# Kernel optimization log

Hardware: AMD Instinct MI355X
Metric: run time of the kernel (lower is better)

## Reference

```python
import jax, jax.numpy as jnp
import numpy as np

B, H, S, D = 4, 16, 1024, 64

def setup_inputs() -> dict:
    key = jax.random.key(0)
    kq, kk, kv, kb, km = jax.random.split(key, 5)
    return {
        "q": jax.random.normal(kq, (B, H, S, D), dtype=jnp.float32),
        "k": jax.random.normal(kk, (B, H, S, D), dtype=jnp.float32),
        "v": jax.random.normal(kv, (B, H, S, D), dtype=jnp.float32),
        "add_attn": jax.random.normal(kb, (B, 1, S, S), dtype=jnp.float32),
        "mask": jax.random.randint(km, (B, 1, 1, S), 0, 2, dtype=jnp.int32),
    }

def reference(q, k, v, add_attn, mask):
    d_emb = q.shape[-1]
    scale = 1.0 / jnp.sqrt(jnp.float32(d_emb)).astype(q.dtype)
    # scores: [B,H,Sq,Sk]
    attn = jnp.einsum('bhqd,bhkd->bhqk', q * scale, k)
    attn = attn + add_attn
    attn = jnp.where(mask == 0, jnp.asarray(-1e9, attn.dtype), attn)
    attn = jax.nn.softmax(attn, axis=-1)  # dropout with p=0 is identity
    output = jnp.einsum('bhqk,bhkd->bhqd', attn, v)
    return (output, attn)
```

## Files before the change

### kernel.cpp

```cpp
#include <hip/hip_runtime.h>
#include <math.h>

#define BB 4
#define HH 16
#define SS 1024
#define DD 64
#define QT 16
#define NKW 4
#define KPW 256
#define HPB 4
#define PTL 264
#define OSTR 68

typedef __attribute__((ext_vector_type(8))) short bf16x8;
typedef __attribute__((ext_vector_type(4))) float f32x4;
typedef __attribute__((ext_vector_type(4))) int   i32x4;

static __device__ inline unsigned short f2bf(float f) {
    unsigned int u = __float_as_uint(f);
    u += 0x7fff + ((u >> 16) & 1);
    return (unsigned short)(u >> 16);
}

__global__ __launch_bounds__(256) void convert_qk(const float* __restrict__ q,
                                                  const float* __restrict__ k,
                                                  unsigned short* __restrict__ qb,
                                                  unsigned short* __restrict__ kb) {
    const int idx = blockIdx.x * 256 + threadIdx.x;
    float4 qv = ((const float4*)q)[idx];
    float4 kv = ((const float4*)k)[idx];
    ushort4 qo = make_ushort4(f2bf(qv.x), f2bf(qv.y), f2bf(qv.z), f2bf(qv.w));
    ushort4 ko = make_ushort4(f2bf(kv.x), f2bf(kv.y), f2bf(kv.z), f2bf(kv.w));
    ((ushort4*)qb)[idx] = qo;
    ((ushort4*)kb)[idx] = ko;
}

__global__ __launch_bounds__(256) void transpose_v(const float* __restrict__ v,
                                                   unsigned short* __restrict__ vt) {
    __shared__ unsigned short t[DD][258];
    const int bh = blockIdx.y;
    const int k0 = blockIdx.x * 256;
    const float* vb = v + ((size_t)bh * SS + k0) * DD;
#pragma unroll
    for (int j = 0; j < 16; ++j) {
        const int f   = j * 256 + threadIdx.x;
        const int row = f >> 4;
        const int d4  = (f & 15) << 2;
        float4 x = ((const float4*)vb)[f];
        t[d4 + 0][row] = f2bf(x.x);
        t[d4 + 1][row] = f2bf(x.y);
        t[d4 + 2][row] = f2bf(x.z);
        t[d4 + 3][row] = f2bf(x.w);
    }
    __syncthreads();
    unsigned short* vo = vt + (size_t)bh * DD * SS + k0;
#pragma unroll
    for (int j = 0; j < 8; ++j) {
        const int f  = j * 256 + threadIdx.x;
        const int d  = f >> 5;
        const int k8 = (f & 31) << 3;
        const unsigned int* lp = (const unsigned int*)&t[d][k8];
        uint4 w;
        w.x = lp[0]; w.y = lp[1]; w.z = lp[2]; w.w = lp[3];
        *(uint4*)(vo + (size_t)d * SS + k8) = w;
    }
}

__global__ __launch_bounds__(256, 2) void attn_mfma(
    const unsigned short* __restrict__ qb,
    const unsigned short* __restrict__ kb,
    const unsigned short* __restrict__ vtb,
    const float* __restrict__ add_attn,
    const int*   __restrict__ mask,
    float* __restrict__ out,
    float* __restrict__ attn_out)
{
    const int P    = blockIdx.x;
    const int xcd  = P & 7;
    const int slot = P >> 3;
    const int hg   = slot & 3;
    const int g    = ((slot >> 2) << 3) | xcd;
    const int qt   = g & 63;
    const int b    = g >> 6;

    const int tid  = threadIdx.x;
    const int wave = tid >> 6;
    const int lane = tid & 63;
    const int col  = lane & 15;
    const int quad = lane >> 4;

    __shared__ unsigned short p_tile[NKW][QT][PTL];
    __shared__ float a_stage[NKW][4][264];
    __shared__ float red_m[NKW][QT];
    __shared__ float red_l[NKW][QT];
    float* o_w = (float*)&p_tile[wave][0][0];

    const int q0  = qt * QT;
    const int wk0 = wave * KPW;

    const float* brow = add_attn + ((size_t)b * SS + q0 + col) * SS;
    const int*   mrow = mask + b * SS;
    float br[16][4];
#pragma unroll
    for (int t = 0; t < 16; ++t) {
        const int kof = wk0 + t * 16 + quad * 4;
        const f32x4 bv = *(const f32x4*)(brow + kof);
        const i32x4 mv = *(const i32x4*)(mrow + kof);
#pragma unroll
        for (int r = 0; r < 4; ++r)
            br[t][r] = mv[r] ? bv[r] : -1e9f;
    }

    for (int hi = 0; hi < HPB; ++hi) {
        const int bh = b * HH + hg * HPB + hi;

        const unsigned short* qrow = qb + ((size_t)bh * SS + q0 + col) * DD + quad * 8;
        const bf16x8 bq0 = *(const bf16x8*)(qrow);
        const bf16x8 bq1 = *(const bf16x8*)(qrow + 32);

        const unsigned short* kbb = kb + (size_t)bh * SS * DD;

        float s[16][4];
#pragma unroll
        for (int t = 0; t < 16; ++t) {
            const unsigned short* kr = kbb + (size_t)(wk0 + t * 16 + col) * DD + quad * 8;
            bf16x8 ak0 = *(const bf16x8*)(kr);
            bf16x8 ak1 = *(const bf16x8*)(kr + 32);
            f32x4 acc = {0.f, 0.f, 0.f, 0.f};
            acc = __builtin_amdgcn_mfma_f32_16x16x32_bf16(ak0, bq0, acc, 0, 0, 0);
            acc = __builtin_amdgcn_mfma_f32_16x16x32_bf16(ak1, bq1, acc, 0, 0, 0);
#pragma unroll
            for (int r = 0; r < 4; ++r)
                s[t][r] = acc[r] * 0.125f + br[t][r];
        }

        float m = s[0][0];
#pragma unroll
        for (int t = 0; t < 16; ++t)
#pragma unroll
            for (int r = 0; r < 4; ++r) m = fmaxf(m, s[t][r]);
        m = fmaxf(m, __shfl_xor(m, 16));
        m = fmaxf(m, __shfl_xor(m, 32));

        float l = 0.f;
#pragma unroll
        for (int t = 0; t < 16; ++t)
#pragma unroll
            for (int r = 0; r < 4; ++r) {
                float e = __expf(s[t][r] - m);
                s[t][r] = e;
                l += e;
            }
        l += __shfl_xor(l, 16);
        l += __shfl_xor(l, 32);

        if (quad == 0) { red_m[wave][col] = m; red_l[wave][col] = l; }
        __syncthreads();

        const float m0 = red_m[0][col], m1 = red_m[1][col];
        const float m2 = red_m[2][col], m3 = red_m[3][col];
        const float gm = fmaxf(fmaxf(m0, m1), fmaxf(m2, m3));
        const float L  = red_l[0][col] * __expf(m0 - gm) +
                         red_l[1][col] * __expf(m1 - gm) +
                         red_l[2][col] * __expf(m2 - gm) +
                         red_l[3][col] * __expf(m3 - gm);
        const float sc = __expf(m - gm) / L;

#pragma unroll
        for (int t = 0; t < 16; ++t) {
            ushort4 pk;
#pragma unroll
            for (int r = 0; r < 4; ++r) {
                const float p = s[t][r] * sc;
                s[t][r] = p;
                ((unsigned short*)&pk)[r] = f2bf(p);
            }
            *(ushort4*)&p_tile[wave][col][t * 16 + quad * 4] = pk;
        }

        float* arow0 = attn_out + ((size_t)bh * SS + q0) * SS + wk0;
#pragma unroll
        for (int gg = 0; gg < 4; ++gg) {
            if ((col >> 2) == gg) {
                const int rr = col & 3;
#pragma unroll
                for (int t = 0; t < 16; ++t) {
                    f32x4 d;
                    d[0] = s[t][0]; d[1] = s[t][1]; d[2] = s[t][2]; d[3] = s[t][3];
                    *(f32x4*)&a_stage[wave][rr][t * 16 + quad * 4] = d;
                }
            }
            asm volatile("s_waitcnt lgkmcnt(0)" ::: "memory");
#pragma unroll
            for (int rr = 0; rr < 4; ++rr) {
                f32x4 d = *(const f32x4*)&a_stage[wave][rr][lane * 4];
                *(f32x4*)(arow0 + (size_t)(gg * 4 + rr) * SS + lane * 4) = d;
            }
        }

        const unsigned short* vt = vtb + (size_t)bh * DD * SS;
        f32x4 oacc[4];
#pragma unroll
        for (int dc = 0; dc < 4; ++dc) oacc[dc] = (f32x4){0.f, 0.f, 0.f, 0.f};
#pragma unroll
        for (int c = 0; c < 8; ++c) {
            bf16x8 ap = *(const bf16x8*)(&p_tile[wave][col][c * 32 + quad * 8]);
#pragma unroll
            for (int dc = 0; dc < 4; ++dc) {
                const unsigned short* vr =
                    vt + (size_t)(dc * 16 + col) * SS + wk0 + c * 32 + quad * 8;
                bf16x8 av = *(const bf16x8*)(vr);
                oacc[dc] = __builtin_amdgcn_mfma_f32_16x16x32_bf16(av, ap, oacc[dc], 0, 0, 0);
            }
        }
#pragma unroll
        for (int dc = 0; dc < 4; ++dc)
            *(f32x4*)(o_w + col * OSTR + dc * 16 + quad * 4) = oacc[dc];
        __syncthreads();

        {
            const int qr = tid >> 4;
            const int d0 = (tid & 15) << 2;
            const float* ob = (const float*)&p_tile[0][0][0];
            const int ws = QT * PTL / 2;
            f32x4 a0 = *(const f32x4*)(ob + 0 * ws + qr * OSTR + d0);
            f32x4 a1 = *(const f32x4*)(ob + 1 * ws + qr * OSTR + d0);
            f32x4 a2 = *(const f32x4*)(ob + 2 * ws + qr * OSTR + d0);
            f32x4 a3 = *(const f32x4*)(ob + 3 * ws + qr * OSTR + d0);
            f32x4 o4 = a0 + a1 + a2 + a3;
            *(f32x4*)(out + ((size_t)bh * SS + q0 + qr) * DD + d0) = o4;
        }
        __syncthreads();
    }
}

extern "C" void kernel_launch(void* const* d_in, const int* in_sizes, int n_in,
                              void* d_out, int out_size, void* d_ws, size_t ws_size,
                              hipStream_t stream) {
    const float* q        = (const float*)d_in[0];
    const float* k        = (const float*)d_in[1];
    const float* v        = (const float*)d_in[2];
    const float* add_attn = (const float*)d_in[3];
    const int*   mask     = (const int*)d_in[4];

    float* out      = (float*)d_out;
    float* attn_out = (float*)d_out + (size_t)BB * HH * SS * DD;

    const size_t nelem = (size_t)BB * HH * SS * DD;
    unsigned short* qb  = (unsigned short*)d_ws;
    unsigned short* kbb = qb + nelem;
    unsigned short* vtb = kbb + nelem;

    convert_qk<<<dim3(nelem / 4 / 256), dim3(256), 0, stream>>>(q, k, qb, kbb);
    transpose_v<<<dim3(SS / 256, BB * HH), dim3(256), 0, stream>>>(v, vtb);

    attn_mfma<<<dim3(SS / QT * (HH / HPB) * BB), dim3(256), 0, stream>>>(
        qb, kbb, vtb, add_attn, mask, out, attn_out);
}
```

Measured before the change: 451.7 us.

## Alias attention staging buffer into P tile and defer attn stores after PV

Drops the separate a_stage shared buffer and reuses each wave's P-tile region for staging attention-probability rows and the partial O tile, which cuts LDS per block and may allow more resident blocks per CU. The attention-matrix global stores move to after the PV MFMA loop, so the store traffic can overlap with the reduction phase. __syncthreads is replaced by an explicit lgkm wait plus s_barrier. The O staging stride changes from 68 to 66 floats, which leaves 16-byte LDS accesses misaligned on odd rows and may split or slow those accesses.

Result: no change. 451.6 us (-0.0%).

```diff
diff --git a/kernel.cpp b/kernel.cpp
--- a/kernel.cpp
+++ b/kernel.cpp
@@ -10,7 +10,7 @@
 #define KPW 256
 #define HPB 4
 #define PTL 264
-#define OSTR 68
+#define OSTR 66
 
 typedef __attribute__((ext_vector_type(8))) short bf16x8;
 typedef __attribute__((ext_vector_type(4))) float f32x4;
@@ -20,6 +20,11 @@
     unsigned int u = __float_as_uint(f);
     u += 0x7fff + ((u >> 16) & 1);
     return (unsigned short)(u >> 16);
+}
+
+static __device__ __forceinline__ void bar_lgkm() {
+    asm volatile("s_waitcnt lgkmcnt(0)" ::: "memory");
+    __builtin_amdgcn_s_barrier();
 }
 
 __global__ __launch_bounds__(256) void convert_qk(const float* __restrict__ q,
@@ -90,10 +95,10 @@
     const int quad = lane >> 4;
 
     __shared__ unsigned short p_tile[NKW][QT][PTL];
-    __shared__ float a_stage[NKW][4][264];
     __shared__ float red_m[NKW][QT];
     __shared__ float red_l[NKW][QT];
-    float* o_w = (float*)&p_tile[wave][0][0];
+    float* wbase = (float*)&p_tile[wave][0][0];
+    float* o_w   = wbase + 1056;
 
     const int q0  = qt * QT;
     const int wk0 = wave * KPW;
@@ -155,7 +160,7 @@
         l += __shfl_xor(l, 32);
 
         if (quad == 0) { red_m[wave][col] = m; red_l[wave][col] = l; }
-        __syncthreads();
+        bar_lgkm();
 
         const float m0 = red_m[0][col], m1 = red_m[1][col];
         const float m2 = red_m[2][col], m3 = red_m[3][col];
@@ -177,26 +182,7 @@
             }
             *(ushort4*)&p_tile[wave][col][t * 16 + quad * 4] = pk;
         }
-
-        float* arow0 = attn_out + ((size_t)bh * SS + q0) * SS + wk0;
-#pragma unroll
-        for (int gg = 0; gg < 4; ++gg) {
-            if ((col >> 2) == gg) {
-                const int rr = col & 3;
-#pragma unroll
-                for (int t = 0; t < 16; ++t) {
-                    f32x4 d;
-                    d[0] = s[t][0]; d[1] = s[t][1]; d[2] = s[t][2]; d[3] = s[t][3];
-                    *(f32x4*)&a_stage[wave][rr][t * 16 + quad * 4] = d;
-                }
-            }
-            asm volatile("s_waitcnt lgkmcnt(0)" ::: "memory");
-#pragma unroll
-            for (int rr = 0; rr < 4; ++rr) {
-                f32x4 d = *(const f32x4*)&a_stage[wave][rr][lane * 4];
-                *(f32x4*)(arow0 + (size_t)(gg * 4 + rr) * SS + lane * 4) = d;
-            }
-        }
+        asm volatile("s_waitcnt lgkmcnt(0)" ::: "memory");
 
         const unsigned short* vt = vtb + (size_t)bh * DD * SS;
         f32x4 oacc[4];
@@ -213,24 +199,50 @@
                 oacc[dc] = __builtin_amdgcn_mfma_f32_16x16x32_bf16(av, ap, oacc[dc], 0, 0, 0);
             }
         }
+        asm volatile("s_waitcnt lgkmcnt(0)" ::: "memory");
+
 #pragma unroll
         for (int dc = 0; dc < 4; ++dc)
             *(f32x4*)(o_w + col * OSTR + dc * 16 + quad * 4) = oacc[dc];
-        __syncthreads();
+
+        {
+            float* arow0 = attn_out + ((size_t)bh * SS + q0) * SS + wk0;
+            float (*a_st)[264] = (float(*)[264])wbase;
+#pragma unroll
+            for (int gg = 0; gg < 4; ++gg) {
+                if ((col >> 2) == gg) {
+                    const int rr = col & 3;
+#pragma unroll
+                    for (int t = 0; t < 16; ++t) {
+                        f32x4 d;
+                        d[0] = s[t][0]; d[1] = s[t][1];
+                        d[2] = s[t][2]; d[3] = s[t][3];
+                        *(f32x4*)&a_st[rr][t * 16 + quad * 4] = d;
+                    }
+                }
+                asm volatile("s_waitcnt lgkmcnt(0)" ::: "memory");
+#pragma unroll
+                for (int rr = 0; rr < 4; ++rr) {
+                    f32x4 d = *(const f32x4*)&a_st[rr][lane * 4];
+                    *(f32x4*)(arow0 + (size_t)(gg * 4 + rr) * SS + lane * 4) = d;
+                }
+            }
+        }
+        bar_lgkm();
 
         {
             const int qr = tid >> 4;
             const int d0 = (tid & 15) << 2;
             const float* ob = (const float*)&p_tile[0][0][0];
             const int ws = QT * PTL / 2;
-            f32x4 a0 = *(const f32x4*)(ob + 0 * ws + qr * OSTR + d0);
-            f32x4 a1 = *(const f32x4*)(ob + 1 * ws + qr * OSTR + d0);
-            f32x4 a2 = *(const f32x4*)(ob + 2 * ws + qr * OSTR + d0);
-            f32x4 a3 = *(const f32x4*)(ob + 3 * ws + qr * OSTR + d0);
+            f32x4 a0 = *(const f32x4*)(ob + 0 * ws + 1056 + qr * OSTR + d0);
+            f32x4 a1 = *(const f32x4*)(ob + 1 * ws + 1056 + qr * OSTR + d0);
+            f32x4 a2 = *(const f32x4*)(ob + 2 * ws + 1056 + qr * OSTR + d0);
+            f32x4 a3 = *(const f32x4*)(ob + 3 * ws + 1056 + qr * OSTR + d0);
             f32x4 o4 = a0 + a1 + a2 + a3;
             *(f32x4*)(out + ((size_t)bh * SS + q0 + qr) * DD + d0) = o4;
         }
-        __syncthreads();
+        bar_lgkm();
     }
 }
 
```
